# Kernel tuning notes

Hardware: AMD Instinct MI355X
Metric: run time of the kernel (lower is better)

The kernel has to match this reference:

```python
import jax, jax.numpy as jnp
import numpy as np
from jax import lax

EPS = 1e-5


def ste_sign(w):
    # deterministic BinaryConnect binarization: sign(w) forward, identity (STE) backward
    return w + lax.stop_gradient(jnp.sign(w) - w)


def bconv(x, w, b):
    y = lax.conv_general_dilated(x, ste_sign(w), (1, 1), 'VALID',
                                 dimension_numbers=('NCHW', 'OIHW', 'NCHW'))
    return y + b[None, :, None, None]


def bn(x, g, be, m, v):
    inv = g * lax.rsqrt(v + EPS)
    return x * inv[None, :, None, None] + (be - m * inv)[None, :, None, None]


def pool(x):
    return lax.reduce_window(x, -jnp.inf, lax.max, (1, 1, 2, 2), (1, 1, 2, 2), 'VALID')


def blinear(x, w, b):
    return x @ ste_sign(w).T + b


def setup_inputs() -> dict:
    key = jax.random.key(0)
    ks = iter(jax.random.split(key, 64))
    d = {}
    d['x'] = jax.random.normal(next(ks), (512, 3, 32, 32), jnp.float32)
    chans = [(128, 3), (128, 128), (256, 128), (256, 256), (512, 256), (512, 512)]
    for i, (co, ci) in enumerate(chans, start=1):
        d[f'w{i}'] = jax.random.normal(next(ks), (co, ci, 3, 3), jnp.float32) * 0.1
        d[f'b{i}'] = jax.random.normal(next(ks), (co,), jnp.float32) * 0.1
        d[f'g{i}'] = jax.random.uniform(next(ks), (co,), jnp.float32) + 0.5
        d[f'be{i}'] = jax.random.normal(next(ks), (co,), jnp.float32) * 0.1
        d[f'm{i}'] = jax.random.normal(next(ks), (co,), jnp.float32) * 0.1
        d[f'v{i}'] = jax.random.uniform(next(ks), (co,), jnp.float32) + 0.5
    d['fw1'] = jax.random.normal(next(ks), (1024, 512), jnp.float32) * 0.05
    d['fb1'] = jax.random.normal(next(ks), (1024,), jnp.float32) * 0.05
    d['fw2'] = jax.random.normal(next(ks), (1024, 1024), jnp.float32) * 0.05
    d['fb2'] = jax.random.normal(next(ks), (1024,), jnp.float32) * 0.05
    d['fw3'] = jax.random.normal(next(ks), (10, 1024), jnp.float32) * 0.05
    d['fb3'] = jax.random.normal(next(ks), (10,), jnp.float32) * 0.05
    return d


def reference(x,
              w1, b1, g1, be1, m1, v1,
              w2, b2, g2, be2, m2, v2,
              w3, b3, g3, be3, m3, v3,
              w4, b4, g4, be4, m4, v4,
              w5, b5, g5, be5, m5, v5,
              w6, b6, g6, be6, m6, v6,
              fw1, fb1, fw2, fb2, fw3, fb3):
    relu = jax.nn.relu
    x = relu(bn(bconv(x, w1, b1), g1, be1, m1, v1))   # [B,128,30,30]
    x = relu(bn(bconv(x, w2, b2), g2, be2, m2, v2))   # [B,128,28,28]
    x = pool(x)                                        # [B,128,14,14]
    x = relu(bn(bconv(x, w3, b3), g3, be3, m3, v3))   # [B,256,12,12]
    x = relu(bn(bconv(x, w4, b4), g4, be4, m4, v4))   # [B,256,10,10]
    x = pool(x)                                        # [B,256,5,5]
    x = relu(bn(bconv(x, w5, b5), g5, be5, m5, v5))   # [B,512,3,3]
    x = relu(bn(bconv(x, w6, b6), g6, be6, m6, v6))   # [B,512,1,1]
    x = x.reshape(x.shape[0], -1)                      # [B,512]
    x = relu(blinear(x, fw1, fb1))
    x = relu(blinear(x, fw2, fb2))
    x = blinear(x, fw3, fb3)
    return jax.nn.softmax(x, axis=1)
```

## Files before the change

### kernel.cpp

```cpp
#include <hip/hip_runtime.h>
#include <math.h>

#define EPS 1e-5f

typedef unsigned short u16;
typedef unsigned int u32;
typedef __attribute__((ext_vector_type(8))) short short8b;
typedef __attribute__((ext_vector_type(4))) float f32x4;

static inline int cdiv(long long a, int b) { return (int)((a + b - 1) / b); }

__device__ __forceinline__ float sgnf(float w) {
    return (w > 0.f) ? 1.f : ((w < 0.f) ? -1.f : 0.f);
}

__device__ __forceinline__ u16 bf16_rne(float v) {
    u32 u = __float_as_uint(v);
    return (u16)((u + 0x7FFFu + ((u >> 16) & 1u)) >> 16);
}
__device__ __forceinline__ void split_bf16(float v, u16& h, u16& l) {
    h = bf16_rne(v);
    float hf = __uint_as_float((u32)h << 16);
    l = bf16_rne(v - hf);
}


__global__ void prep_conv_w(const float* __restrict__ w, float* __restrict__ wst,
                            int CO, int CI)
{
    int idx = blockIdx.x * blockDim.x + threadIdx.x;
    int n = CO * CI * 9;
    if (idx >= n) return;
    int k  = idx % 9;
    int ci = (idx / 9) % CI;
    int co = idx / (9 * CI);
    wst[((((co >> 4) * CI + ci) * 9 + k) << 4) + (co & 15)] = sgnf(w[idx]);
}

__global__ void prep_wfrag(const float* __restrict__ w, u16* __restrict__ wB,
                           int CO, int CI)
{
    int idx = blockIdx.x * blockDim.x + threadIdx.x;
    int n = CO * CI * 9;
    if (idx >= n) return;
    int tap = idx % 9;
    int ci  = (idx / 9) % CI;
    int co  = idx / (9 * CI);
    int CIS = CI >> 5;
    int ncg = co >> 4;
    int l   = (co & 15) | (((ci >> 3) & 3) << 4);
    int j   = ci & 7;
    int cis = ci >> 5;
    size_t off = (((size_t)(ncg * 9 + tap) * CIS + cis) * 64 + l) * 8 + j;
    float wv = w[idx];
    wB[off] = wv > 0.f ? (u16)0x3F80 : (wv < 0.f ? (u16)0xBF80 : (u16)0);
}

__global__ void prep_gemm_wfrag(const float* __restrict__ w, u16* __restrict__ frag,
                                int OUT, int K, int OUTP, int mode)
{
    long long idx = (long long)blockIdx.x * blockDim.x + threadIdx.x;
    long long n = (long long)OUTP * K;
    if (idx >= n) return;
    int k = (int)(idx % K);
    int o = (int)(idx / K);
    u16 b = 0;
    if (o < OUT) {
        float wv;
        if (mode == 1) {
            int ci = k & 511, tap = k >> 9;
            wv = w[((size_t)o * 512 + ci) * 9 + tap];
        } else {
            wv = w[(size_t)o * K + k];
        }
        b = wv > 0.f ? (u16)0x3F80 : (wv < 0.f ? (u16)0xBF80 : (u16)0);
    }
    int KS = K >> 5;
    int ncg = o >> 4;
    int lane = (o & 15) | (((k >> 3) & 3) << 4);
    int j = k & 7, ks = k >> 5;
    frag[((size_t)(ncg * KS + ks) * 64 + lane) * 8 + j] = b;
}

__global__ void bn_prep(const float* __restrict__ bias, const float* __restrict__ g,
                        const float* __restrict__ be, const float* __restrict__ m,
                        const float* __restrict__ v,
                        float* __restrict__ sc, float* __restrict__ sh, int CO)
{
    int i = blockIdx.x * blockDim.x + threadIdx.x;
    if (i >= CO) return;
    float s = g[i] * rsqrtf(v[i] + EPS);
    sc[i] = s;
    sh[i] = be[i] - m[i] * s + bias[i] * s;
}

template<int CI, int CO, int IH, int TMR, int MSPW, int OUTMODE>
__global__ __launch_bounds__(256) void conv_mfma_halo(
    const u16* __restrict__ xhi, const u16* __restrict__ xlo,
    const u16* __restrict__ wB,
    const float* __restrict__ scale, const float* __restrict__ shift,
    float* __restrict__ yf, u16* __restrict__ yhi, u16* __restrict__ ylo)
{
    constexpr int IW = IH, OH = IH - 2, OW = OH, PLANE = OH * OW, IPLANE = IH * IW;
    constexpr int TM = TMR * OW;
    constexpr int TILES = PLANE / TM;
    static_assert(PLANE % TM == 0, "tile");
    constexpr int PX = (TMR + 2) * IW;
    constexpr int CIS = CI / 32;
    constexpr int NSUB = (TM + 15) / 16;
    static_assert(NSUB <= 4 * MSPW, "slots");
    static_assert(OUTMODE != 2 || (TMR % 2 == 0 && OW % 2 == 0), "pool");
    constexpr int NBN = CO / 128;
    constexpr int PLB = PX * 64;
    constexpr int PWT = OW / 2;
    constexpr int NQ  = (TMR / 2) * PWT;
    constexpr int PPLANE = (OH / 2) * (OW / 2);

    __shared__ __align__(16) u16 As[2 * PX * 32];

    const int gid  = blockIdx.x;
    const int nb   = gid % NBN;
    const int tw   = gid / NBN;
    const int simg = tw / TILES;
    const int tile = tw - simg * TILES;
    const int ncg0 = nb * 8;
    const int t = threadIdx.x, lane = t & 63, wv = t >> 6;
    const long long gpix0 = (long long)simg * IPLANE + (long long)tile * TMR * IW;

    int lpb[MSPW];
    #pragma unroll
    for (int s = 0; s < MSPW; ++s) {
        int st = wv * MSPW + s;
        int m = st * 16 + (lane & 15);
        if constexpr (OUTMODE == 2) {
            int q = m >> 2, r = m & 3;
            if (q > NQ - 1) q = NQ - 1;
            int pr = q / PWT, pc = q - pr * PWT;
            lpb[s] = (2 * pr + (r >> 1)) * IW + 2 * pc + (r & 1);
        } else {
            int p = (m > TM - 1) ? (TM - 1) : m;
            int pr = p / OW, pc = p - pr * OW;
            lpb[s] = pr * IW + pc;
        }
    }

    f32x4 acc[MSPW][8];
    #pragma unroll
    for (int s = 0; s < MSPW; ++s)
        #pragma unroll
        for (int n = 0; n < 8; ++n)
            #pragma unroll
            for (int r = 0; r < 4; ++r)
                acc[s][n][r] = 0.f;

    for (int cs = 0; cs < CIS; ++cs) {
        if (cs) __syncthreads();
        for (int u = t; u < PX * 8; u += 256) {
            int lp = u >> 3, sub = u & 7, pl = sub >> 2, cib = sub & 3;
            const u16* sp = pl ? xlo : xhi;
            uint4 v = *(const uint4*)(sp + (gpix0 + lp) * CI + (cs << 5) + (cib << 3));
            *(uint4*)((char*)As + pl * PLB + lp * 64 + ((cib ^ ((lp >> 1) & 3)) << 4)) = v;
        }
        __syncthreads();
        #pragma unroll
        for (int tap = 0; tap < 9; ++tap) {
            const int kh = tap / 3, kw = tap - 3 * (tap / 3);
            short8b bfr[8];
            #pragma unroll
            for (int n = 0; n < 8; ++n)
                bfr[n] = *(const short8b*)(wB +
                    (((size_t)((ncg0 + n) * 9 + tap) * CIS + cs) << 9) + (lane << 3));
            #pragma unroll
            for (int s = 0; s < MSPW; ++s) {
                const int lp  = lpb[s] + kh * IW + kw;
                const int off = lp * 64 + (((lane >> 4) ^ ((lp >> 1) & 3)) << 4);
                short8b ah = *(const short8b*)((char*)As + off);
                short8b al = *(const short8b*)((char*)As + PLB + off);
                #pragma unroll
                for (int n = 0; n < 8; ++n) {
                    acc[s][n] = __builtin_amdgcn_mfma_f32_16x16x32_bf16(ah, bfr[n], acc[s][n], 0, 0, 0);
                    acc[s][n] = __builtin_amdgcn_mfma_f32_16x16x32_bf16(al, bfr[n], acc[s][n], 0, 0, 0);
                }
            }
        }
    }

    const int mrow = (lane >> 4) << 2;
    #pragma unroll
    for (int s = 0; s < MSPW; ++s) {
        const int st = wv * MSPW + s;
        if constexpr (OUTMODE == 2) {
            int q = st * 4 + (lane >> 4);
            if (q > NQ - 1) q = NQ - 1;
            const int pr = q / PWT, pc = q - pr * PWT;
            const int gq = (tile * (TMR / 2) + pr) * PWT + pc;
            #pragma unroll
            for (int n = 0; n < 8; ++n) {
                const int co = ((ncg0 + n) << 4) + (lane & 15);
                const float sc_ = scale[co], sh_ = shift[co];
                float vmax = 0.f;
                #pragma unroll
                for (int r = 0; r < 4; ++r) {
                    float val = fmaxf(fmaf(acc[s][n][r], sc_, sh_), 0.f);
                    vmax = fmaxf(vmax, val);
                }
                const size_t o = ((size_t)simg * PPLANE + gq) * CO + co;
                u16 h, l; split_bf16(vmax, h, l);
                yhi[o] = h; ylo[o] = l;
            }
        } else {
            #pragma unroll
            for (int n = 0; n < 8; ++n) {
                const int co = ((ncg0 + n) << 4) + (lane & 15);
                const float sc_ = scale[co], sh_ = shift[co];
                #pragma unroll
                for (int r = 0; r < 4; ++r) {
                    const int pl_ = st * 16 + mrow + r;
                    if (pl_ < TM) {
                        float val = fmaxf(fmaf(acc[s][n][r], sc_, sh_), 0.f);
                        const size_t o = ((size_t)simg * PLANE + (size_t)tile * TM + pl_) * CO + co;
                        if constexpr (OUTMODE == 1) {
                            u16 h, l; split_bf16(val, h, l);
                            yhi[o] = h; ylo[o] = l;
                        } else {
                            yf[o] = val;
                        }
                    }
                }
            }
        }
    }
}

template<int CI, int CO, int IH, int HILO_OUT>
__global__ __launch_bounds__(256) void conv_mfma(
    const u16* __restrict__ xhi, const u16* __restrict__ xlo,
    const u16* __restrict__ wB,
    const float* __restrict__ scale, const float* __restrict__ shift,
    float* __restrict__ yf, u16* __restrict__ yhi, u16* __restrict__ ylo,
    int M_total, int NB_N)
{
    constexpr int IW = IH, OH = IH - 2, OW = IH - 2, PLANE = OH * OW;
    constexpr int CIS = CI / 32;
    __shared__ __align__(16) u16 As[2 * 128 * 32];

    const int bid = blockIdx.x;
    const int nb  = bid % NB_N;
    const int mb  = bid / NB_N;
    const int ncg0 = nb * 8;
    const int t    = threadIdx.x;
    const int lane = t & 63;
    const int wv   = t >> 6;

    const int sp  = t >> 1;
    const int P_s = mb * 128 + sp;
    const int Pc  = (P_s < M_total) ? P_s : 0;
    const int simg = Pc / PLANE;
    const int sp2  = Pc - simg * PLANE;
    const int soh  = sp2 / OW;
    const int sow  = sp2 - soh * OW;
    const int sbase = (simg * IH + soh) * IW + sow;
    const int sh16  = (t & 1) << 4;
    const int swz   = (sp >> 1) & 3;
    char* Ab  = (char*)As;
    char* wA0 = Ab + sp * 64 + (((((t & 1) << 1)    ) ^ swz) << 4);
    char* wA1 = Ab + sp * 64 + (((((t & 1) << 1) | 1) ^ swz) << 4);

    const int pix0  = (wv << 5) + (lane & 15);
    const int roff0 = pix0 * 64 + (((lane >> 4) ^ ((pix0 >> 1) & 3)) << 4);

    f32x4 acc[2][8];
    #pragma unroll
    for (int i = 0; i < 2; ++i)
        #pragma unroll
        for (int j = 0; j < 8; ++j)
            #pragma unroll
            for (int r = 0; r < 4; ++r)
                acc[i][j][r] = 0.f;

    for (int tap = 0; tap < 9; ++tap) {
        const int koff = (tap / 3) * IW + (tap - (tap / 3) * 3);
        for (int cs = 0; cs < CIS; ++cs) {
            if (tap | cs) __syncthreads();
            {
                const int g = (sbase + koff) * CI + (cs << 5) + sh16;
                uint4 h0 = *(const uint4*)(xhi + g);
                uint4 h1 = *(const uint4*)(xhi + g + 8);
                uint4 l0 = *(const uint4*)(xlo + g);
                uint4 l1 = *(const uint4*)(xlo + g + 8);
                *(uint4*)(wA0)        = h0;
                *(uint4*)(wA1)        = h1;
                *(uint4*)(wA0 + 8192) = l0;
                *(uint4*)(wA1 + 8192) = l1;
            }
            __syncthreads();

            short8b bfr[8];
            #pragma unroll
            for (int n = 0; n < 8; ++n) {
                const u16* wp = wB + (((size_t)((ncg0 + n) * 9 + tap) * CIS + cs) << 9)
                                   + (lane << 3);
                bfr[n] = *(const short8b*)wp;
            }
            #pragma unroll
            for (int hl = 0; hl < 2; ++hl) {
                short8b a0 = *(const short8b*)(Ab + hl * 8192 + roff0);
                short8b a1 = *(const short8b*)(Ab + hl * 8192 + roff0 + 1024);
                #pragma unroll
                for (int n = 0; n < 8; ++n) {
                    acc[0][n] = __builtin_amdgcn_mfma_f32_16x16x32_bf16(a0, bfr[n], acc[0][n], 0, 0, 0);
                    acc[1][n] = __builtin_amdgcn_mfma_f32_16x16x32_bf16(a1, bfr[n], acc[1][n], 0, 0, 0);
                }
            }
        }
    }

    const int mrow = (lane >> 4) << 2;
    #pragma unroll
    for (int mt = 0; mt < 2; ++mt) {
        const int Pb = mb * 128 + ((wv * 2 + mt) << 4) + mrow;
        #pragma unroll
        for (int n = 0; n < 8; ++n) {
            const int co = ((ncg0 + n) << 4) + (lane & 15);
            const float sc_ = scale[co], sh_ = shift[co];
            #pragma unroll
            for (int r = 0; r < 4; ++r) {
                const int P = Pb + r;
                if (P < M_total) {
                    float val = fmaxf(fmaf(acc[mt][n][r], sc_, sh_), 0.f);
                    const size_t o = (size_t)P * CO + co;
                    if constexpr (HILO_OUT) {
                        u16 h, l; split_bf16(val, h, l);
                        yhi[o] = h; ylo[o] = l;
                    } else {
                        yf[o] = val;
                    }
                }
            }
        }
    }
}

template<int N_REP>
__global__ __launch_bounds__(256) void fc_mfma_split(
    const u16* __restrict__ Ahi, const u16* __restrict__ Alo,
    const u16* __restrict__ wB, float* __restrict__ part,
    int M, int K, int NB_N, int KSC)
{
    __shared__ __align__(16) u16 As[2 * 128 * 32];
    const int KS = K >> 5;
    const int MB = M >> 7;
    const int Npad = NB_N * N_REP * 16;
    const int bid = blockIdx.x;
    const int nb  = bid % NB_N;
    int tmp = bid / NB_N;
    const int mb    = tmp % MB;
    const int split = tmp / MB;
    const int ks0 = split * KSC;
    const int ks1 = (ks0 + KSC < KS) ? (ks0 + KSC) : KS;
    const int ncg0 = nb * N_REP;
    const int t    = threadIdx.x;
    const int lane = t & 63;
    const int wv   = t >> 6;

    const int sp = t >> 1;
    int srow = mb * 128 + sp;
    if (srow >= M) srow = M - 1;
    const size_t abase = (size_t)srow * K + ((t & 1) << 4);
    const int swz = (sp >> 1) & 3;
    char* Ab  = (char*)As;
    char* wA0 = Ab + sp * 64 + (((((t & 1) << 1)    ) ^ swz) << 4);
    char* wA1 = Ab + sp * 64 + (((((t & 1) << 1) | 1) ^ swz) << 4);

    const int pix0  = (wv << 5) + (lane & 15);
    const int roff0 = pix0 * 64 + (((lane >> 4) ^ ((pix0 >> 1) & 3)) << 4);

    f32x4 acc[2][N_REP];
    #pragma unroll
    for (int i = 0; i < 2; ++i)
        #pragma unroll
        for (int j = 0; j < N_REP; ++j)
            #pragma unroll
            for (int r = 0; r < 4; ++r)
                acc[i][j][r] = 0.f;

    for (int ks = ks0; ks < ks1; ++ks) {
        if (ks != ks0) __syncthreads();
        {
            const size_t g = abase + ((size_t)ks << 5);
            uint4 h0 = *(const uint4*)(Ahi + g);
            uint4 h1 = *(const uint4*)(Ahi + g + 8);
            uint4 l0 = *(const uint4*)(Alo + g);
            uint4 l1 = *(const uint4*)(Alo + g + 8);
            *(uint4*)(wA0)        = h0;
            *(uint4*)(wA1)        = h1;
            *(uint4*)(wA0 + 8192) = l0;
            *(uint4*)(wA1 + 8192) = l1;
        }
        __syncthreads();

        short8b bfr[N_REP];
        #pragma unroll
        for (int n = 0; n < N_REP; ++n)
            bfr[n] = *(const short8b*)(wB + ((size_t)(ncg0 + n) * KS + ks) * 512
                                          + (lane << 3));
        #pragma unroll
        for (int hl = 0; hl < 2; ++hl) {
            short8b a0 = *(const short8b*)(Ab + hl * 8192 + roff0);
            short8b a1 = *(const short8b*)(Ab + hl * 8192 + roff0 + 1024);
            #pragma unroll
            for (int n = 0; n < N_REP; ++n) {
                acc[0][n] = __builtin_amdgcn_mfma_f32_16x16x32_bf16(a0, bfr[n], acc[0][n], 0, 0, 0);
                acc[1][n] = __builtin_amdgcn_mfma_f32_16x16x32_bf16(a1, bfr[n], acc[1][n], 0, 0, 0);
            }
        }
    }

    const int mrow = (lane >> 4) << 2;
    #pragma unroll
    for (int mt = 0; mt < 2; ++mt) {
        const int Pb = mb * 128 + ((wv * 2 + mt) << 4) + mrow;
        #pragma unroll
        for (int n = 0; n < N_REP; ++n) {
            const int co = ((ncg0 + n) << 4) + (lane & 15);
            #pragma unroll
            for (int r = 0; r < 4; ++r) {
                const int P = Pb + r;
                if (P < M)
                    part[((size_t)split * M + P) * Npad + co] = acc[mt][n][r];
            }
        }
    }
}

template<int HILO_OUT>
__global__ void fc_reduce(const float* __restrict__ part, int nsplit,
                          const float* __restrict__ sc, const float* __restrict__ sh,
                          float* __restrict__ yf, u16* __restrict__ yhi,
                          u16* __restrict__ ylo,
                          int M, int Nact, int Npad, int relu)
{
    int idx = blockIdx.x * blockDim.x + threadIdx.x;
    if (idx >= M * Nact) return;
    int n = idx % Nact, m = idx / Nact;
    float s = 0.f;
    for (int k = 0; k < nsplit; ++k)
        s += part[((size_t)k * M + m) * Npad + n];
    float val = fmaf(s, sc ? sc[n] : 1.f, sh[n]);
    if (relu) val = fmaxf(val, 0.f);
    if constexpr (HILO_OUT) {
        u16 h, l; split_bf16(val, h, l);
        yhi[idx] = h; ylo[idx] = l;
    } else {
        yf[idx] = val;
    }
}

template<int CI, int CI_T, int IMGS, int NT, int IH, int CO, int HILO_OUT>
__global__ __launch_bounds__(NT) void conv_tiled(
    const float* __restrict__ x, const float* __restrict__ wst,
    const float* __restrict__ scale, const float* __restrict__ shift,
    float* __restrict__ y, u16* __restrict__ yhi, u16* __restrict__ ylo,
    int Btot)
{
    constexpr int IW = IH;
    constexpr int OH = IH - 2, OW = IW - 2;
    constexpr int PLANE  = OH * OW;
    constexpr int IPLANE = IH * IW;
    constexpr int NPIX = IMGS * PLANE;
    constexpr int LDSZ = IMGS * CI_T * IPLANE;
    constexpr int LDS4 = LDSZ / 4;
    constexpr int SLAB4 = CI_T * IPLANE / 4;
    constexpr int IMG_STRIDE4 = CI * IPLANE / 4;
    constexpr int NTILE = CI / CI_T;
    constexpr int NCG = CO / 16;
    constexpr int LOG2_NCG = (NCG == 8) ? 3 : ((NCG == 16) ? 4 : 5);
    static_assert(NPIX <= NT, "thread count too small");
    static_assert((CI_T * IPLANE) % 4 == 0 && (CI * IPLANE) % 4 == 0, "f4");

    __shared__ __align__(16) float xs[LDSZ];

    const int nim = (Btot + IMGS - 1) / IMGS;
    int n = blockIdx.x;
    int cg, ig;
    if ((nim & 7) == 0) {
        int xcd = n & 7;
        int w   = n >> 3;
        cg = w & (NCG - 1);
        ig = xcd + ((w >> LOG2_NCG) << 3);
    } else {
        cg = n & (NCG - 1);
        ig = n >> LOG2_NCG;
    }

    const int b0 = ig * IMGS;
    const int t  = threadIdx.x;

    const int tc  = (t < NPIX) ? t : (NPIX - 1);
    const int img = tc / PLANE;
    const int pix = tc - img * PLANE;
    const int oh  = pix / OW;
    const int ow  = pix - oh * OW;
    const bool act = (t < NPIX) && (b0 + img < Btot);

    float acc[16];
    #pragma unroll
    for (int q = 0; q < 16; ++q) acc[q] = 0.f;

    const int xbase = (img * CI_T * IH + oh) * IW + ow;

    for (int ct = 0; ct < NTILE; ++ct) {
        if (ct) __syncthreads();
        {
            const float4* xsrc = (const float4*)(x +
                ((long long)b0 * CI + (long long)ct * CI_T) * IPLANE);
            for (int j = t; j < LDS4; j += NT) {
                int im, r;
                if constexpr (IMGS == 1) { im = 0; r = j; }
                else { im = j / SLAB4; r = j - im * SLAB4; }
                float4 val = make_float4(0.f, 0.f, 0.f, 0.f);
                if (b0 + im < Btot) val = xsrc[(long long)im * IMG_STRIDE4 + r];
                ((float4*)xs)[j] = val;
            }
        }
        __syncthreads();
        const float* wt = wst + ((long long)(cg * CI + ct * CI_T) * 9) * 16;
        for (int ci = 0; ci < CI_T; ++ci) {
            const float* xr = xs + xbase + ci * IPLANE;
            const float* wr = wt + ci * 144;
            #pragma unroll
            for (int kh = 0; kh < 3; ++kh) {
                float x0 = xr[kh * IW + 0];
                float x1 = xr[kh * IW + 1];
                float x2 = xr[kh * IW + 2];
                const float* wk = wr + kh * 48;
                #pragma unroll
                for (int q = 0; q < 16; ++q) acc[q] = fmaf(x0, wk[q],      acc[q]);
                #pragma unroll
                for (int q = 0; q < 16; ++q) acc[q] = fmaf(x1, wk[16 + q], acc[q]);
                #pragma unroll
                for (int q = 0; q < 16; ++q) acc[q] = fmaf(x2, wk[32 + q], acc[q]);
            }
        }
    }

    if (act) {
        const int co0 = cg * 16;
        if constexpr (HILO_OUT) {
            const size_t o = ((size_t)(b0 + img) * PLANE + pix) * (size_t)CO + co0;
            u32* ohp = (u32*)(yhi + o);
            u32* olp = (u32*)(ylo + o);
            #pragma unroll
            for (int qq = 0; qq < 8; ++qq) {
                float v0 = fmaxf(fmaf(acc[2*qq],   scale[co0+2*qq],   shift[co0+2*qq]),   0.f);
                float v1 = fmaxf(fmaf(acc[2*qq+1], scale[co0+2*qq+1], shift[co0+2*qq+1]), 0.f);
                u16 h0, l0, h1, l1;
                split_bf16(v0, h0, l0); split_bf16(v1, h1, l1);
                ohp[qq] = (u32)h0 | ((u32)h1 << 16);
                olp[qq] = (u32)l0 | ((u32)l1 << 16);
            }
        } else {
            float* yp = y + ((long long)(b0 + img) * CO + co0) * PLANE + pix;
            #pragma unroll
            for (int q = 0; q < 16; ++q) {
                float val = fmaf(acc[q], scale[co0 + q], shift[co0 + q]);
                yp[(long long)q * PLANE] = fmaxf(val, 0.f);
            }
        }
    }
}

__global__ void softmax10_kernel(const float* __restrict__ logits,
                                 float* __restrict__ out, int B)
{
    int b = blockIdx.x * blockDim.x + threadIdx.x;
    if (b >= B) return;
    float l[10];
    float mx = -1e30f;
    #pragma unroll
    for (int i = 0; i < 10; ++i) { l[i] = logits[b * 10 + i]; mx = fmaxf(mx, l[i]); }
    float s = 0.f;
    #pragma unroll
    for (int i = 0; i < 10; ++i) { l[i] = __expf(l[i] - mx); s += l[i]; }
    float r = 1.f / s;
    #pragma unroll
    for (int i = 0; i < 10; ++i) out[b * 10 + i] = l[i] * r;
}

extern "C" void kernel_launch(void* const* d_in, const int* in_sizes, int n_in,
                              void* d_out, int out_size, void* d_ws, size_t ws_size,
                              hipStream_t stream)
{
    const int B = 512;
    const float* x = (const float*)d_in[0];
    auto W  = [&](int i) { return (const float*)d_in[1 + (i - 1) * 6 + 0]; };
    auto Bi = [&](int i) { return (const float*)d_in[1 + (i - 1) * 6 + 1]; };
    auto G  = [&](int i) { return (const float*)d_in[1 + (i - 1) * 6 + 2]; };
    auto Be = [&](int i) { return (const float*)d_in[1 + (i - 1) * 6 + 3]; };
    auto M  = [&](int i) { return (const float*)d_in[1 + (i - 1) * 6 + 4]; };
    auto V  = [&](int i) { return (const float*)d_in[1 + (i - 1) * 6 + 5]; };
    const float* fw1 = (const float*)d_in[37];
    const float* fb1 = (const float*)d_in[38];
    const float* fw2 = (const float*)d_in[39];
    const float* fb2 = (const float*)d_in[40];
    const float* fw3 = (const float*)d_in[41];
    const float* fb3 = (const float*)d_in[42];
    float* out = (float*)d_out;

    char* pb = (char*)d_ws;
    auto takeB = [&](long long nb) { char* r = pb; pb += (nb + 255) & ~255LL; return r; };
    float* wst1 = (float*)takeB(128LL * 3 * 9 * 4);
    u16*   wB2  = (u16*)takeB(128LL * 128 * 9 * 2);
    u16*   wB3  = (u16*)takeB(256LL * 128 * 9 * 2);
    u16*   wB4  = (u16*)takeB(256LL * 256 * 9 * 2);
    u16*   wB5  = (u16*)takeB(512LL * 256 * 9 * 2);
    u16*   wB6  = (u16*)takeB(512LL * 4608 * 2);
    u16*   wF1  = (u16*)takeB(1024LL * 512 * 2);
    u16*   wF2  = (u16*)takeB(1024LL * 1024 * 2);
    u16*   wF3  = (u16*)takeB(16LL * 1024 * 2);
    const int COs[6] = {128, 128, 256, 256, 512, 512};
    float* SC[6]; float* SH[6];
    for (int i = 0; i < 6; ++i) {
        SC[i] = (float*)takeB(COs[i] * 4);
        SH[i] = (float*)takeB(COs[i] * 4);
    }
    u16* y5hi = (u16*)takeB(512LL * 4608 * 2);
    u16* y5lo = (u16*)takeB(512LL * 4608 * 2);
    u16* t6hi = (u16*)takeB(512LL * 512 * 2);
    u16* t6lo = (u16*)takeB(512LL * 512 * 2);
    u16* f1hi = (u16*)takeB(512LL * 1024 * 2);
    u16* f1lo = (u16*)takeB(512LL * 1024 * 2);
    u16* f2hi = (u16*)takeB(512LL * 1024 * 2);
    u16* f2lo = (u16*)takeB(512LL * 1024 * 2);
    float* logits = (float*)takeB(512LL * 10 * 4);
    float* fcpart = (float*)takeB(16LL * 512 * 512 * 4);
    long long wbytes = pb - (char*)d_ws;

    const long long A_PER_B = 460800, B_PER_B = 100352;
    int Bc = B;
    while (Bc > 64 && wbytes + (long long)Bc * (A_PER_B + B_PER_B) > (long long)ws_size)
        Bc >>= 1;
    char* regionA = takeB((long long)Bc * A_PER_B);
    char* regionB = takeB((long long)Bc * B_PER_B);

    const int TB = 256;

    prep_conv_w<<<cdiv(128LL * 3 * 9, TB), TB, 0, stream>>>(W(1), wst1, 128, 3);
    prep_wfrag<<<cdiv(128LL * 128 * 9, TB), TB, 0, stream>>>(W(2), wB2, 128, 128);
    prep_wfrag<<<cdiv(256LL * 128 * 9, TB), TB, 0, stream>>>(W(3), wB3, 256, 128);
    prep_wfrag<<<cdiv(256LL * 256 * 9, TB), TB, 0, stream>>>(W(4), wB4, 256, 256);
    prep_wfrag<<<cdiv(512LL * 256 * 9, TB), TB, 0, stream>>>(W(5), wB5, 512, 256);
    prep_gemm_wfrag<<<cdiv(512LL * 4608, TB), TB, 0, stream>>>(W(6), wB6, 512, 4608, 512, 1);
    prep_gemm_wfrag<<<cdiv(1024LL * 512, TB), TB, 0, stream>>>(fw1, wF1, 1024, 512, 1024, 0);
    prep_gemm_wfrag<<<cdiv(1024LL * 1024, TB), TB, 0, stream>>>(fw2, wF2, 1024, 1024, 1024, 0);
    prep_gemm_wfrag<<<cdiv(16LL * 1024, TB), TB, 0, stream>>>(fw3, wF3, 10, 1024, 16, 0);
    for (int i = 0; i < 6; ++i)
        bn_prep<<<cdiv(COs[i], TB), TB, 0, stream>>>(Bi(i + 1), G(i + 1), Be(i + 1),
                                                     M(i + 1), V(i + 1), SC[i], SH[i], COs[i]);

    for (int b0 = 0; b0 < B; b0 += Bc) {
        int bc = (B - b0 < Bc) ? (B - b0) : Bc;
        const float* xc = x + (long long)b0 * 3 * 32 * 32;

        u16* a1hi = (u16*)regionA;
        u16* a1lo = a1hi + (size_t)Bc * 115200;
        u16* a2hi = (u16*)regionB;
        u16* a2lo = a2hi + (size_t)Bc * 25088;
        u16* a3hi = (u16*)regionA;
        u16* a3lo = a3hi + (size_t)Bc * 36864;
        u16* a4hi = (u16*)regionB;
        u16* a4lo = a4hi + (size_t)Bc * 6400;

        conv_tiled<3, 3, 1, 960, 32, 128, 1>
            <<<8 * bc, 960, 0, stream>>>(xc, wst1, SC[0], SH[0], nullptr, a1hi, a1lo, bc);

        conv_mfma_halo<128, 128, 30, 4, 2, 2><<<bc * 7, 256, 0, stream>>>(
            a1hi, a1lo, wB2, SC[1], SH[1], nullptr, a2hi, a2lo);

        conv_mfma_halo<128, 256, 14, 12, 3, 1><<<bc * 2, 256, 0, stream>>>(
            a2hi, a2lo, wB3, SC[2], SH[2], nullptr, a3hi, a3lo);

        conv_mfma_halo<256, 256, 12, 10, 2, 2><<<bc * 2, 256, 0, stream>>>(
            a3hi, a3lo, wB4, SC[3], SH[3], nullptr, a4hi, a4lo);

        int M5 = bc * 9;
        conv_mfma<256, 512, 5, 1><<<cdiv(M5, 128) * 4, 256, 0, stream>>>(
            a4hi, a4lo, wB5, SC[4], SH[4], nullptr,
            y5hi + (size_t)b0 * 4608, y5lo + (size_t)b0 * 4608, M5, 4);
    }

    fc_mfma_split<8><<<256, 256, 0, stream>>>(y5hi, y5lo, wB6, fcpart, 512, 4608, 4, 9);
    fc_reduce<1><<<cdiv(512LL * 512, TB), TB, 0, stream>>>(
        fcpart, 16, SC[5], SH[5], nullptr, t6hi, t6lo, 512, 512, 512, 1);
    fc_mfma_split<8><<<256, 256, 0, stream>>>(t6hi, t6lo, wF1, fcpart, 512, 512, 8, 2);
    fc_reduce<1><<<cdiv(512LL * 1024, TB), TB, 0, stream>>>(
        fcpart, 8, nullptr, fb1, nullptr, f1hi, f1lo, 512, 1024, 1024, 1);
    fc_mfma_split<8><<<256, 256, 0, stream>>>(f1hi, f1lo, wF2, fcpart, 512, 1024, 8, 4);
    fc_reduce<1><<<cdiv(512LL * 1024, TB), TB, 0, stream>>>(
        fcpart, 8, nullptr, fb2, nullptr, f2hi, f2lo, 512, 1024, 1024, 1);
    fc_mfma_split<1><<<64, 256, 0, stream>>>(f2hi, f2lo, wF3, fcpart, 512, 1024, 1, 2);
    fc_reduce<0><<<cdiv(512LL * 10, TB), TB, 0, stream>>>(
        fcpart, 16, nullptr, fb3, logits, nullptr, nullptr, 512, 10, 16, 0);
    softmax10_kernel<<<cdiv(512LL, TB), TB, 0, stream>>>(logits, out, 512);
}
```

Measured before the change: 978.3 us.

## Double-buffer conv input tiles with register-staged prefetch of next channel slice

The halo conv kernel now holds two LDS buffers. Global loads for the next 32-channel slice are issued into registers before the MFMA loop over the current slice, then written to the other buffer afterwards. This removes one barrier per slice and hides global load latency behind the MFMA work. In exchange it doubles LDS use and adds staging registers, which could lower occupancy or cause spills given the large accumulator arrays.

```diff
diff --git a/kernel.cpp b/kernel.cpp
--- a/kernel.cpp
+++ b/kernel.cpp
@@ -112,11 +112,13 @@
     static_assert(OUTMODE != 2 || (TMR % 2 == 0 && OW % 2 == 0), "pool");
     constexpr int NBN = CO / 128;
     constexpr int PLB = PX * 64;
+    constexpr int BUFB = 2 * PLB;
+    constexpr int NLD = (PX * 8 + 255) / 256;
     constexpr int PWT = OW / 2;
     constexpr int NQ  = (TMR / 2) * PWT;
     constexpr int PPLANE = (OH / 2) * (OW / 2);
 
-    __shared__ __align__(16) u16 As[2 * PX * 32];
+    __shared__ __align__(16) u16 As[2 * 2 * PX * 32];
 
     const int gid  = blockIdx.x;
     const int nb   = gid % NBN;
@@ -153,15 +155,39 @@
             for (int r = 0; r < 4; ++r)
                 acc[s][n][r] = 0.f;
 
+    uint4 stg[NLD];
+    auto issue = [&](int cs) {
+        #pragma unroll
+        for (int i = 0; i < NLD; ++i) {
+            int u = t + i * 256;
+            if (u < PX * 8) {
+                int lp = u >> 3, sub = u & 7, pl = sub >> 2, cib = sub & 3;
+                const u16* sp = pl ? xlo : xhi;
+                stg[i] = *(const uint4*)(sp + (gpix0 + lp) * CI + (cs << 5) + (cib << 3));
+            }
+        }
+    };
+    auto commit = [&](int buf) {
+        #pragma unroll
+        for (int i = 0; i < NLD; ++i) {
+            int u = t + i * 256;
+            if (u < PX * 8) {
+                int lp = u >> 3, sub = u & 7, pl = sub >> 2, cib = sub & 3;
+                *(uint4*)((char*)As + buf * BUFB + pl * PLB + lp * 64 +
+                          ((cib ^ ((lp >> 1) & 3)) << 4)) = stg[i];
+            }
+        }
+    };
+
+    issue(0);
+    commit(0);
+    __syncthreads();
+
     for (int cs = 0; cs < CIS; ++cs) {
-        if (cs) __syncthreads();
-        for (int u = t; u < PX * 8; u += 256) {
-            int lp = u >> 3, sub = u & 7, pl = sub >> 2, cib = sub & 3;
-            const u16* sp = pl ? xlo : xhi;
-            uint4 v = *(const uint4*)(sp + (gpix0 + lp) * CI + (cs << 5) + (cib << 3));
-            *(uint4*)((char*)As + pl * PLB + lp * 64 + ((cib ^ ((lp >> 1) & 3)) << 4)) = v;
-        }
-        __syncthreads();
+        const int cur = cs & 1;
+        const bool more = (cs + 1 < CIS);
+        if (more) issue(cs + 1);
+        const char* Ab = (char*)As + cur * BUFB;
         #pragma unroll
         for (int tap = 0; tap < 9; ++tap) {
             const int kh = tap / 3, kw = tap - 3 * (tap / 3);
@@ -174,14 +200,18 @@
             for (int s = 0; s < MSPW; ++s) {
                 const int lp  = lpb[s] + kh * IW + kw;
                 const int off = lp * 64 + (((lane >> 4) ^ ((lp >> 1) & 3)) << 4);
-                short8b ah = *(const short8b*)((char*)As + off);
-                short8b al = *(const short8b*)((char*)As + PLB + off);
+                short8b ah = *(const short8b*)(Ab + off);
+                short8b al = *(const short8b*)(Ab + PLB + off);
                 #pragma unroll
                 for (int n = 0; n < 8; ++n) {
                     acc[s][n] = __builtin_amdgcn_mfma_f32_16x16x32_bf16(ah, bfr[n], acc[s][n], 0, 0, 0);
                     acc[s][n] = __builtin_amdgcn_mfma_f32_16x16x32_bf16(al, bfr[n], acc[s][n], 0, 0, 0);
                 }
             }
+        }
+        if (more) {
+            commit(cur ^ 1);
+            __syncthreads();
         }
     }
 
```

Result: slower. 1.206 ms (+23.3%).
